# Kernel tuning notes

Hardware: AMD Instinct MI355X
Metric: run time of the kernel (lower is better)

## Reference

```python
import jax, jax.numpy as jnp
import numpy as np

D_MODEL = 2048
N_HEADS = 16
D_K = D_MODEL // N_HEADS
BATCH = 2
SEQ = 2048


def _rope(q, k):
    # q,k: [B, H, S, Dk], interleaved even/odd RoPE as in the torch source
    seq_len = q.shape[2]
    d = q.shape[-1]
    freqs = 1.0 / (10000.0 ** (jnp.arange(0, d, 2.0, dtype=jnp.float32) / d))  # [Dk/2]
    pos = jnp.arange(seq_len, dtype=jnp.float32)
    ang = pos[:, None] * freqs[None, :]          # [S, Dk/2]
    sin, cos = jnp.sin(ang), jnp.cos(ang)

    def rot(t):
        te, to = t[..., ::2], t[..., 1::2]
        out = jnp.stack([te * cos - to * sin, te * sin + to * cos], axis=-1)
        return out.reshape(t.shape)

    return rot(q), rot(k)


def setup_inputs() -> dict:
    key = jax.random.key(0)
    ks = jax.random.split(key, 5)
    scale = 1.0 / np.sqrt(D_MODEL)
    return {
        "x": jax.random.normal(ks[0], (BATCH, SEQ, D_MODEL), jnp.float32),
        "w_q": jax.random.normal(ks[1], (D_MODEL, D_MODEL), jnp.float32) * scale,
        "w_k": jax.random.normal(ks[2], (D_MODEL, D_MODEL), jnp.float32) * scale,
        "w_v": jax.random.normal(ks[3], (D_MODEL, D_MODEL), jnp.float32) * scale,
        "w_o": jax.random.normal(ks[4], (D_MODEL, D_MODEL), jnp.float32) * scale,
        "b_o": jnp.zeros((D_MODEL,), jnp.float32),
    }


def reference(x, w_q, w_k, w_v, w_o, b_o):
    B, S, D = x.shape
    H, Dk = N_HEADS, D_K
    # nn.Linear: y = x @ W.T
    q = (x @ w_q.T).reshape(B, S, H, Dk).transpose(0, 2, 1, 3)
    k = (x @ w_k.T).reshape(B, S, H, Dk).transpose(0, 2, 1, 3)
    v = (x @ w_v.T).reshape(B, S, H, Dk).transpose(0, 2, 1, 3)
    q, k = _rope(q, k)
    scores = jnp.einsum('bhqd,bhkd->bhqk', q, k) / jnp.sqrt(jnp.float32(Dk))
    causal = jnp.tril(jnp.ones((S, S), bool))  # True = keep
    scores = jnp.where(causal[None, None], scores, -jnp.inf)
    attn = jax.nn.softmax(scores, axis=-1)
    out = jnp.einsum('bhqk,bhkd->bhqd', attn, v)
    out = out.transpose(0, 2, 1, 3).reshape(B, S, D)
    return out @ w_o.T + b_o
```

## Files before the change

### kernel.cpp

```cpp
#include <hip/hip_runtime.h>

#define D_MODEL 2048
#define NHEADS  16
#define DK      128
#define BATCH   2
#define SEQ     2048
#define MTOT    (BATCH*SEQ)

typedef unsigned short u16;
typedef unsigned int   u32;
typedef __bf16 bf16x8 __attribute__((ext_vector_type(8)));
typedef float  f32x4  __attribute__((ext_vector_type(4)));

__device__ __forceinline__ float b2f(u16 u) {
  return __uint_as_float(((u32)u) << 16);
}
__device__ __forceinline__ u16 f2b(float f) {
  u32 x = __float_as_uint(f);
  x += 0x7fffu + ((x >> 16) & 1u);
  return (u16)(x >> 16);
}

__device__ __forceinline__ void gl2lds16(const u16* g, u16* l) {
  __builtin_amdgcn_global_load_lds(
      (const __attribute__((address_space(1))) void*)g,
      (__attribute__((address_space(3))) void*)l, 16, 0, 0);
}

__global__ __launch_bounds__(256) void cvt_k(const float* __restrict__ in,
                                             u16* __restrict__ out, int n4) {
  int i = blockIdx.x * 256 + threadIdx.x;
  if (i >= n4) return;
  float4 v = ((const float4*)in)[i];
  u32 lo = (u32)f2b(v.x) | ((u32)f2b(v.y) << 16);
  u32 hi = (u32)f2b(v.z) | ((u32)f2b(v.w) << 16);
  ((uint2*)out)[i] = make_uint2(lo, hi);
}

__global__ __launch_bounds__(256) void cvt4_k(const float* __restrict__ a, const float* __restrict__ b,
                                              const float* __restrict__ c, const float* __restrict__ d,
                                              u16* __restrict__ oa, u16* __restrict__ ob,
                                              u16* __restrict__ oc, u16* __restrict__ od, int n4) {
  int z = blockIdx.y;
  const float* in = (z == 0) ? a : (z == 1) ? b : (z == 2) ? c : d;
  u16* out = (z == 0) ? oa : (z == 1) ? ob : (z == 2) ? oc : od;
  int i = blockIdx.x * 256 + threadIdx.x;
  if (i >= n4) return;
  float4 v = ((const float4*)in)[i];
  u32 lo = (u32)f2b(v.x) | ((u32)f2b(v.y) << 16);
  u32 hi = (u32)f2b(v.z) | ((u32)f2b(v.w) << 16);
  ((uint2*)out)[i] = make_uint2(lo, hi);
}

__global__ __launch_bounds__(512, 2) void gemm256(const u16* __restrict__ A,
                                                  const u16* __restrict__ B,
                                                  const int M, const int N, const int K,
                                                  u16* __restrict__ outb,
                                                  float* __restrict__ outf,
                                                  const float* __restrict__ bias,
                                                  const int mode) {
  __shared__ __align__(16) u16 smem[3 * 24576];

  const int t    = threadIdx.x;
  const int lane = t & 63;
  const int wave = t >> 6;
  const int wm   = wave >> 1, wn = wave & 1;
  const int quad = lane >> 4, l16 = lane & 15;
  const int m0 = blockIdx.y * 256, n0 = blockIdx.x * 128;
  const int sr = lane & 15, sc = lane >> 4;

  const u16* agp[4]; u16* ald[4];
  const u16* bgp[2]; u16* bld[2];
#pragma unroll
  for (int q = 0; q < 4; ++q) {
    int a = wave * 4 + q;
    int kc = a >> 4, mt = a & 15;
    agp[q] = A + (size_t)(m0 + mt * 16 + sr) * K + kc * 32 + sc * 8;
    ald[q] = smem + a * 512;
  }
#pragma unroll
  for (int q = 0; q < 2; ++q) {
    int b = wave * 2 + q;
    int kc = b >> 3, nt = b & 7;
    bgp[q] = B + (size_t)(n0 + nt * 16 + sr) * K + kc * 32 + sc * 8;
    bld[q] = smem + 16384 + b * 512;
  }

  f32x4 acc[4][4] = {};
  const int NT = K >> 6;

#pragma unroll
  for (int q = 0; q < 4; ++q) { gl2lds16(agp[q], ald[q]);         agp[q] += 64; }
#pragma unroll
  for (int q = 0; q < 2; ++q) { gl2lds16(bgp[q], bld[q]);         bgp[q] += 64; }
#pragma unroll
  for (int q = 0; q < 4; ++q) { gl2lds16(agp[q], ald[q] + 24576); agp[q] += 64; }
#pragma unroll
  for (int q = 0; q < 2; ++q) { gl2lds16(bgp[q], bld[q] + 24576); bgp[q] += 64; }

  int cur = 0;
  for (int tt = 0; tt < NT; ++tt) {
    if (tt + 1 < NT) asm volatile("s_waitcnt vmcnt(6)" ::: "memory");
    else             asm volatile("s_waitcnt vmcnt(0)" ::: "memory");
    __builtin_amdgcn_s_barrier();
    asm volatile("" ::: "memory");

    if (tt + 2 < NT) {
      int nb = cur + 2; if (nb >= 3) nb -= 3;
      const int off = nb * 24576;
#pragma unroll
      for (int q = 0; q < 4; ++q) { gl2lds16(agp[q], ald[q] + off); agp[q] += 64; }
#pragma unroll
      for (int q = 0; q < 2; ++q) { gl2lds16(bgp[q], bld[q] + off); bgp[q] += 64; }
    }

    const u16* As = smem + cur * 24576;
    const u16* Bs = As + 16384;
#pragma unroll
    for (int kc = 0; kc < 2; ++kc) {
      bf16x8 af[4], bfv[4];
#pragma unroll
      for (int i = 0; i < 4; ++i)
        af[i] = *(const bf16x8*)&As[(kc * 16 + wm * 4 + i) * 512 + lane * 8];
#pragma unroll
      for (int j = 0; j < 4; ++j)
        bfv[j] = *(const bf16x8*)&Bs[(kc * 8 + wn * 4 + j) * 512 + lane * 8];
      __builtin_amdgcn_s_setprio(1);
#pragma unroll
      for (int i = 0; i < 4; ++i)
#pragma unroll
        for (int j = 0; j < 4; ++j)
          acc[i][j] = __builtin_amdgcn_mfma_f32_16x16x32_bf16(af[i], bfv[j], acc[i][j], 0, 0, 0);
      __builtin_amdgcn_s_setprio(0);
    }
    asm volatile("" ::: "memory");
    __builtin_amdgcn_s_barrier();
    cur = cur + 1; if (cur >= 3) cur -= 3;
  }

  if (mode == 0) {
#pragma unroll
    for (int i = 0; i < 4; ++i)
#pragma unroll
      for (int j = 0; j < 4; ++j)
#pragma unroll
        for (int rr = 0; rr < 4; ++rr) {
          int row = m0 + wm * 64 + i * 16 + quad * 4 + rr;
          int col = n0 + wn * 64 + j * 16 + l16;
          outf[(size_t)row * N + col] = acc[i][j][rr] + bias[col];
        }
  } else {
    const int tens = n0 >> 11;
    const int h    = (n0 & 2047) >> 7;
    const bool doRope = (tens < 2);
    const float mult = (tens == 0) ? 0.08838834764831845f : 1.0f;
#pragma unroll
    for (int j = 0; j < 4; ++j) {
      const int d = wn * 64 + j * 16 + l16;
      const float freq = exp2f(-0.20762050593045951f * (float)(d >> 1));
      const float sgn  = (d & 1) ? 1.f : -1.f;
#pragma unroll
      for (int i = 0; i < 4; ++i)
#pragma unroll
        for (int rr = 0; rr < 4; ++rr) {
          int row = m0 + wm * 64 + i * 16 + quad * 4 + rr;
          int b = row >> 11;
          int s = row & (SEQ - 1);
          float v = acc[i][j][rr];
          if (doRope) {
            float sn, cs;
            __sincosf((float)s * freq, &sn, &cs);
            float pv = __shfl_xor(v, 1);
            v = (v * cs + sgn * pv * sn) * mult;
          }
          outb[(size_t)tens * 8388608 + (((size_t)(b * NHEADS + h)) * SEQ + s) * DK + d] = f2b(v);
        }
    }
  }
}

__global__ __launch_bounds__(256) void vt_k(const u16* __restrict__ V,
                                            u16* __restrict__ Vt) {
  constexpr int LDT = 72;
  __shared__ __align__(16) u16 tile[64 * LDT];
  const int s0 = blockIdx.x * 64, d0 = blockIdx.y * 64, bh = blockIdx.z;
  const u16* in = V + (size_t)bh * SEQ * DK;
  u16* out = Vt + (size_t)bh * DK * SEQ;
  const int t = threadIdx.x;
  const int r = t >> 3, cg = t & 7;
#pragma unroll
  for (int half = 0; half < 2; ++half) {
    uint4 v = *(const uint4*)(in + (size_t)(s0 + r + half * 32) * DK + d0 + cg * 8);
    *(uint4*)&tile[(r + half * 32) * LDT + cg * 8] = v;
  }
  __syncthreads();
#pragma unroll
  for (int half = 0; half < 2; ++half) {
    int d = (t >> 3) + half * 32;
    __align__(16) u16 tmp[8];
#pragma unroll
    for (int i = 0; i < 8; ++i) tmp[i] = tile[(cg * 8 + i) * LDT + d];
    *(uint4*)(out + (size_t)(d0 + d) * SEQ + s0 + cg * 8) = *(const uint4*)tmp;
  }
}

__global__ __launch_bounds__(256, 4) void attn_k(const u16* __restrict__ Q,
                                                 const u16* __restrict__ K,
                                                 const u16* __restrict__ Vt,
                                                 u16* __restrict__ out) {
  __shared__ __align__(16) u16 smem[8192 + 8192 + 4096];
  u16* Ks = smem;
  u16* Vs = smem + 8192;

  const int t    = threadIdx.x;
  const int lane = t & 63;
  const int wave = t >> 6;
  const int quad = lane >> 4, l16 = lane & 15;
  u16* Psw = smem + 16384 + wave * 1024;
  const int pmask = (l16 & 7) << 3;
  const int qt = (int)gridDim.x - 1 - (int)blockIdx.x;
  const int bh = blockIdx.y;
  const size_t baseQK = (size_t)bh * SEQ * DK;
  const size_t baseV  = (size_t)bh * DK * SEQ;
  const int qw = qt * 64 + wave * 16;
  const int qglob = qw + l16;

  bf16x8 qf[4];
#pragma unroll
  for (int kc = 0; kc < 4; ++kc)
    qf[kc] = *(const bf16x8*)(Q + baseQK + (size_t)(qw + l16) * DK + kc * 32 + quad * 8);

  f32x4 oacc[8] = {};
  float m_run = -1e30f, l_run = 0.f;

  const int sr = lane & 15, sc = lane >> 4;
  const u16* kp[4]; u16* kd[4];
  const u16* vp[4]; u16* vd[4];
#pragma unroll
  for (int j = 0; j < 4; ++j) {
    int lin = wave * 4 + j;
    int knt = lin >> 2, kkc = lin & 3;
    kp[j] = K + baseQK + (size_t)(knt * 16 + sr) * DK + kkc * 32 + sc * 8;
    kd[j] = Ks + lin * 512;
    int vkc = lin >> 3, vnt = lin & 7;
    vp[j] = Vt + baseV + (size_t)(vnt * 16 + sr) * SEQ + vkc * 32 + sc * 8;
    vd[j] = Vs + lin * 512;
  }

  const int kend = (qt + 1) * 64;
  for (int k0 = 0; k0 < kend; k0 += 64) {
    __syncthreads();
#pragma unroll
    for (int j = 0; j < 4; ++j) gl2lds16(kp[j], kd[j]);
#pragma unroll
    for (int j = 0; j < 4; ++j) gl2lds16(vp[j], vd[j]);
#pragma unroll
    for (int j = 0; j < 4; ++j) { kp[j] += (size_t)64 * DK; vp[j] += 64; }
    __syncthreads();

    if (k0 >= qw + 16) continue;

    f32x4 s[4] = {};
#pragma unroll
    for (int kc = 0; kc < 4; ++kc) {
#pragma unroll
      for (int nt = 0; nt < 4; ++nt) {
        bf16x8 kf = *(const bf16x8*)&Ks[(nt * 4 + kc) * 512 + lane * 8];
        s[nt] = __builtin_amdgcn_mfma_f32_16x16x32_bf16(kf, qf[kc], s[nt], 0, 0, 0);
      }
    }

    float p[4][4];
    float newm = m_run;
    if (k0 + 63 > qw) {
#pragma unroll
      for (int nt = 0; nt < 4; ++nt)
#pragma unroll
        for (int r = 0; r < 4; ++r) {
          int key = k0 + nt * 16 + quad * 4 + r;
          float v = (key <= qglob) ? s[nt][r] : -1e30f;
          p[nt][r] = v;
          newm = fmaxf(newm, v);
        }
    } else {
#pragma unroll
      for (int nt = 0; nt < 4; ++nt)
#pragma unroll
        for (int r = 0; r < 4; ++r) {
          p[nt][r] = s[nt][r];
          newm = fmaxf(newm, s[nt][r]);
        }
    }
    newm = fmaxf(newm, __shfl_xor(newm, 16));
    newm = fmaxf(newm, __shfl_xor(newm, 32));
    float lsum = 0.f;
#pragma unroll
    for (int nt = 0; nt < 4; ++nt)
#pragma unroll
      for (int r = 0; r < 4; ++r) {
        float e = __expf(p[nt][r] - newm);
        p[nt][r] = e;
        lsum += e;
      }
    lsum += __shfl_xor(lsum, 16);
    lsum += __shfl_xor(lsum, 32);
    float alpha = __expf(m_run - newm);
    l_run = l_run * alpha + lsum;
    m_run = newm;

#pragma unroll
    for (int nt = 0; nt < 4; ++nt) {
      u32 lo = (u32)f2b(p[nt][0]) | ((u32)f2b(p[nt][1]) << 16);
      u32 hi = (u32)f2b(p[nt][2]) | ((u32)f2b(p[nt][3]) << 16);
      *(uint2*)&Psw[l16 * 64 + ((nt * 16 + quad * 4) ^ pmask)] = make_uint2(lo, hi);
    }

#pragma unroll
    for (int r = 0; r < 4; ++r) {
      float av = __shfl(alpha, quad * 4 + r);
#pragma unroll
      for (int nt = 0; nt < 8; ++nt) oacc[nt][r] *= av;
    }

#pragma unroll
    for (int kcp = 0; kcp < 2; ++kcp) {
      bf16x8 pf = *(const bf16x8*)&Psw[l16 * 64 + ((kcp * 32 + quad * 8) ^ pmask)];
#pragma unroll
      for (int nt = 0; nt < 8; ++nt) {
        bf16x8 vf = *(const bf16x8*)&Vs[(kcp * 8 + nt) * 512 + lane * 8];
        oacc[nt] = __builtin_amdgcn_mfma_f32_16x16x32_bf16(pf, vf, oacc[nt], 0, 0, 0);
      }
    }
  }

  constexpr int LDO = 136;
  float invl = 1.f / l_run;
  __syncthreads();
#pragma unroll
  for (int r = 0; r < 4; ++r) {
    float iv = __shfl(invl, quad * 4 + r);
#pragma unroll
    for (int nt = 0; nt < 8; ++nt)
      smem[(wave * 16 + quad * 4 + r) * LDO + nt * 16 + l16] = f2b(oacc[nt][r] * iv);
  }
  __syncthreads();
  const int b = bh >> 4, h = bh & 15;
#pragma unroll
  for (int pss = 0; pss < 4; ++pss) {
    int row = (t >> 4) + pss * 16;
    uint4 v = *(const uint4*)&smem[row * LDO + (t & 15) * 8];
    *(uint4*)(out + ((size_t)(b * SEQ + qt * 64 + row)) * D_MODEL + h * DK + (t & 15) * 8) = v;
  }
}

extern "C" void kernel_launch(void* const* d_in, const int* in_sizes, int n_in,
                              void* d_out, int out_size, void* d_ws, size_t ws_size,
                              hipStream_t stream) {
  const float* x  = (const float*)d_in[0];
  const float* wq = (const float*)d_in[1];
  const float* wk = (const float*)d_in[2];
  const float* wv = (const float*)d_in[3];
  const float* wo = (const float*)d_in[4];
  const float* bo = (const float*)d_in[5];
  float* out = (float*)d_out;

  char* wsb = (char*)d_ws;
  u16* xb    = (u16*)(wsb + 0);
  u16* wqb   = (u16*)(wsb + 16777216);
  u16* wkb   = (u16*)(wsb + 25165824);
  u16* wvb   = (u16*)(wsb + 33554432);
  u16* wob   = (u16*)(wsb + 41943040);
  u16* Qb    = (u16*)(wsb + 50331648);
  u16* Kb    = (u16*)(wsb + 67108864);
  u16* Vb    = (u16*)(wsb + 83886080);
  u16* attnb = xb;
  u16* Vtb   = wqb;

  cvt_k<<<8192, 256, 0, stream>>>(x, xb, MTOT * D_MODEL / 4);
  cvt4_k<<<dim3(4096, 4), 256, 0, stream>>>(wq, wk, wv, wo, wqb, wkb, wvb, wob,
                                            D_MODEL * D_MODEL / 4);

  gemm256<<<dim3(48, 16), 512, 0, stream>>>(xb, wqb, MTOT, 3 * D_MODEL, D_MODEL,
                                            Qb, nullptr, nullptr, 1);

  vt_k<<<dim3(SEQ / 64, DK / 64, BATCH * NHEADS), 256, 0, stream>>>(Vb, Vtb);

  attn_k<<<dim3(SEQ / 64, BATCH * NHEADS), 256, 0, stream>>>(Qb, Kb, Vtb, attnb);

  gemm256<<<dim3(16, 16), 512, 0, stream>>>(attnb, wob, MTOT, D_MODEL, D_MODEL,
                                            nullptr, out, bo, 0);
}
```

Before: 492.4 us.

## Switch GEMM to double-buffered half-tile pipeline with split K-chunk loads

Replaces the triple-buffered 64-wide K staging in the bf16 GEMM with a two-buffer scheme that loads and consumes each 32-wide K half separately. Each half-step issues the global-to-LDS loads for the next half right after reading fragments from LDS. Explicit barriers and lgkmcnt waits separate the LDS reads from the MFMA blocks. This cuts LDS use from 144KB to 96KB per block and overlaps copies at finer granularity, at the cost of twice as many barriers per K step and a shallower prefetch distance.

New measurement: 492.9 us. No clear change (+0.1%).

```diff
diff --git a/kernel.cpp b/kernel.cpp
--- a/kernel.cpp
+++ b/kernel.cpp
@@ -59,7 +59,7 @@
                                                   float* __restrict__ outf,
                                                   const float* __restrict__ bias,
                                                   const int mode) {
-  __shared__ __align__(16) u16 smem[3 * 24576];
+  __shared__ __align__(16) u16 smem[2 * 24576];
 
   const int t    = threadIdx.x;
   const int lane = t & 63;
@@ -69,73 +69,87 @@
   const int m0 = blockIdx.y * 256, n0 = blockIdx.x * 128;
   const int sr = lane & 15, sc = lane >> 4;
 
-  const u16* agp[4]; u16* ald[4];
-  const u16* bgp[2]; u16* bld[2];
-#pragma unroll
-  for (int q = 0; q < 4; ++q) {
-    int a = wave * 4 + q;
-    int kc = a >> 4, mt = a & 15;
-    agp[q] = A + (size_t)(m0 + mt * 16 + sr) * K + kc * 32 + sc * 8;
-    ald[q] = smem + a * 512;
-  }
-#pragma unroll
-  for (int q = 0; q < 2; ++q) {
-    int b = wave * 2 + q;
-    int kc = b >> 3, nt = b & 7;
-    bgp[q] = B + (size_t)(n0 + nt * 16 + sr) * K + kc * 32 + sc * 8;
-    bld[q] = smem + 16384 + b * 512;
-  }
+  const u16* aP[2][2]; u32 aOff[2][2];
+  const u16* bP[2];    u32 bOff[2];
+#pragma unroll
+  for (int kc = 0; kc < 2; ++kc) {
+#pragma unroll
+    for (int q = 0; q < 2; ++q) {
+      int mt = wave * 2 + q;
+      aP[kc][q]  = A + (size_t)(m0 + mt * 16 + sr) * K + kc * 32 + sc * 8;
+      aOff[kc][q] = (u32)(kc * 16 + mt) * 512;
+    }
+    bP[kc]  = B + (size_t)(n0 + wave * 16 + sr) * K + kc * 32 + sc * 8;
+    bOff[kc] = 16384u + (u32)(kc * 8 + wave) * 512;
+  }
+
+  auto issueHalf = [&](int kc, int buf) {
+    u16* base = smem + buf * 24576;
+    gl2lds16(aP[kc][0], base + aOff[kc][0]); aP[kc][0] += 64;
+    gl2lds16(aP[kc][1], base + aOff[kc][1]); aP[kc][1] += 64;
+    gl2lds16(bP[kc],    base + bOff[kc]);    bP[kc]    += 64;
+  };
 
   f32x4 acc[4][4] = {};
   const int NT = K >> 6;
 
-#pragma unroll
-  for (int q = 0; q < 4; ++q) { gl2lds16(agp[q], ald[q]);         agp[q] += 64; }
-#pragma unroll
-  for (int q = 0; q < 2; ++q) { gl2lds16(bgp[q], bld[q]);         bgp[q] += 64; }
-#pragma unroll
-  for (int q = 0; q < 4; ++q) { gl2lds16(agp[q], ald[q] + 24576); agp[q] += 64; }
-#pragma unroll
-  for (int q = 0; q < 2; ++q) { gl2lds16(bgp[q], bld[q] + 24576); bgp[q] += 64; }
-
-  int cur = 0;
+  issueHalf(0, 0);
+  issueHalf(1, 0);
+  issueHalf(0, 1);
+  asm volatile("s_waitcnt vmcnt(3)" ::: "memory");
+  __builtin_amdgcn_s_barrier();
+
   for (int tt = 0; tt < NT; ++tt) {
-    if (tt + 1 < NT) asm volatile("s_waitcnt vmcnt(6)" ::: "memory");
-    else             asm volatile("s_waitcnt vmcnt(0)" ::: "memory");
-    __builtin_amdgcn_s_barrier();
-    asm volatile("" ::: "memory");
-
-    if (tt + 2 < NT) {
-      int nb = cur + 2; if (nb >= 3) nb -= 3;
-      const int off = nb * 24576;
-#pragma unroll
-      for (int q = 0; q < 4; ++q) { gl2lds16(agp[q], ald[q] + off); agp[q] += 64; }
-#pragma unroll
-      for (int q = 0; q < 2; ++q) { gl2lds16(bgp[q], bld[q] + off); bgp[q] += 64; }
-    }
-
-    const u16* As = smem + cur * 24576;
+    const int cb = tt & 1;
+    const u16* As = smem + cb * 24576;
     const u16* Bs = As + 16384;
-#pragma unroll
-    for (int kc = 0; kc < 2; ++kc) {
-      bf16x8 af[4], bfv[4];
-#pragma unroll
-      for (int i = 0; i < 4; ++i)
-        af[i] = *(const bf16x8*)&As[(kc * 16 + wm * 4 + i) * 512 + lane * 8];
-#pragma unroll
-      for (int j = 0; j < 4; ++j)
-        bfv[j] = *(const bf16x8*)&Bs[(kc * 8 + wn * 4 + j) * 512 + lane * 8];
-      __builtin_amdgcn_s_setprio(1);
-#pragma unroll
-      for (int i = 0; i < 4; ++i)
-#pragma unroll
-        for (int j = 0; j < 4; ++j)
-          acc[i][j] = __builtin_amdgcn_mfma_f32_16x16x32_bf16(af[i], bfv[j], acc[i][j], 0, 0, 0);
-      __builtin_amdgcn_s_setprio(0);
-    }
+
+    bf16x8 af[4], bfv[4];
+#pragma unroll
+    for (int i = 0; i < 4; ++i)
+      af[i] = *(const bf16x8*)&As[(wm * 4 + i) * 512 + lane * 8];
+#pragma unroll
+    for (int j = 0; j < 4; ++j)
+      bfv[j] = *(const bf16x8*)&Bs[(wn * 4 + j) * 512 + lane * 8];
+    if (tt + 1 < NT) issueHalf(1, cb ^ 1);
     asm volatile("" ::: "memory");
     __builtin_amdgcn_s_barrier();
-    cur = cur + 1; if (cur >= 3) cur -= 3;
+    asm volatile("s_waitcnt lgkmcnt(0)" ::: "memory");
+    __builtin_amdgcn_sched_barrier(0);
+    __builtin_amdgcn_s_setprio(1);
+#pragma unroll
+    for (int i = 0; i < 4; ++i)
+#pragma unroll
+      for (int j = 0; j < 4; ++j)
+        acc[i][j] = __builtin_amdgcn_mfma_f32_16x16x32_bf16(af[i], bfv[j], acc[i][j], 0, 0, 0);
+    __builtin_amdgcn_s_setprio(0);
+    asm volatile("" ::: "memory");
+    __builtin_amdgcn_s_barrier();
+
+#pragma unroll
+    for (int i = 0; i < 4; ++i)
+      af[i] = *(const bf16x8*)&As[(16 + wm * 4 + i) * 512 + lane * 8];
+#pragma unroll
+    for (int j = 0; j < 4; ++j)
+      bfv[j] = *(const bf16x8*)&Bs[(8 + wn * 4 + j) * 512 + lane * 8];
+    if (tt + 2 < NT) issueHalf(0, cb);
+    if (tt + 1 < NT) {
+      if (tt + 2 < NT) asm volatile("s_waitcnt vmcnt(3)" ::: "memory");
+      else             asm volatile("s_waitcnt vmcnt(0)" ::: "memory");
+    }
+    asm volatile("" ::: "memory");
+    __builtin_amdgcn_s_barrier();
+    asm volatile("s_waitcnt lgkmcnt(0)" ::: "memory");
+    __builtin_amdgcn_sched_barrier(0);
+    __builtin_amdgcn_s_setprio(1);
+#pragma unroll
+    for (int i = 0; i < 4; ++i)
+#pragma unroll
+      for (int j = 0; j < 4; ++j)
+        acc[i][j] = __builtin_amdgcn_mfma_f32_16x16x32_bf16(af[i], bfv[j], acc[i][j], 0, 0, 0);
+    __builtin_amdgcn_s_setprio(0);
+    asm volatile("" ::: "memory");
+    __builtin_amdgcn_s_barrier();
   }
 
   if (mode == 0) {
```

## Enlarge GEMM tile to 256x256 with double-buffered, interleaved load/MFMA schedule

Applied to the files above, without the earlier changes.

The bf16 GEMM block tile grows from 256x128 to 256x256, with 8 waves arranged 2x4 and each wave holding 8x4 accumulators. The triple-buffered LDS pipeline becomes a double buffer whose global-to-LDS loads for the next tile are spread across four MFMA phases, with barriers and setprio between them. The aim is more reuse per LDS load and hiding of global-load latency. The cost is twice as many accumulator registers and far fewer blocks: 384 for the QKV projection and only 128 for the output projection, which may underfill the GPU's CUs.

New measurement: 532.3 us. +8.1%, slower.

```diff
diff --git a/kernel.cpp b/kernel.cpp
--- a/kernel.cpp
+++ b/kernel.cpp
@@ -59,111 +59,156 @@
                                                   float* __restrict__ outf,
                                                   const float* __restrict__ bias,
                                                   const int mode) {
-  __shared__ __align__(16) u16 smem[3 * 24576];
+  __shared__ __align__(16) u16 smem[65536];
 
   const int t    = threadIdx.x;
   const int lane = t & 63;
   const int wave = t >> 6;
-  const int wm   = wave >> 1, wn = wave & 1;
+  const int wm   = wave >> 2, wn = wave & 3;
   const int quad = lane >> 4, l16 = lane & 15;
-  const int m0 = blockIdx.y * 256, n0 = blockIdx.x * 128;
+  const int m0 = blockIdx.y * 256, n0 = blockIdx.x * 256;
   const int sr = lane & 15, sc = lane >> 4;
 
-  const u16* agp[4]; u16* ald[4];
-  const u16* bgp[2]; u16* bld[2];
+  const u16* aSrc[4]; u32 aDst[4];
+  const u16* bSrc[4]; u32 bDst[4];
 #pragma unroll
   for (int q = 0; q < 4; ++q) {
-    int a = wave * 4 + q;
-    int kc = a >> 4, mt = a & 15;
-    agp[q] = A + (size_t)(m0 + mt * 16 + sr) * K + kc * 32 + sc * 8;
-    ald[q] = smem + a * 512;
-  }
-#pragma unroll
-  for (int q = 0; q < 2; ++q) {
-    int b = wave * 2 + q;
-    int kc = b >> 3, nt = b & 7;
-    bgp[q] = B + (size_t)(n0 + nt * 16 + sr) * K + kc * 32 + sc * 8;
-    bld[q] = smem + 16384 + b * 512;
-  }
-
-  f32x4 acc[4][4] = {};
+    int id = q * 8 + wave;
+    int kc = id >> 4, t16 = id & 15;
+    aSrc[q] = A + (size_t)(m0 + t16 * 16 + sr) * K + kc * 32 + sc * 8;
+    aDst[q] = (u32)id * 512;
+    bSrc[q] = B + (size_t)(n0 + t16 * 16 + sr) * K + kc * 32 + sc * 8;
+    bDst[q] = 16384u + (u32)id * 512;
+  }
+
+  f32x4 acc[8][4] = {};
   const int NT = K >> 6;
 
 #pragma unroll
-  for (int q = 0; q < 4; ++q) { gl2lds16(agp[q], ald[q]);         agp[q] += 64; }
-#pragma unroll
-  for (int q = 0; q < 2; ++q) { gl2lds16(bgp[q], bld[q]);         bgp[q] += 64; }
-#pragma unroll
-  for (int q = 0; q < 4; ++q) { gl2lds16(agp[q], ald[q] + 24576); agp[q] += 64; }
-#pragma unroll
-  for (int q = 0; q < 2; ++q) { gl2lds16(bgp[q], bld[q] + 24576); bgp[q] += 64; }
-
-  int cur = 0;
+  for (int q = 0; q < 4; ++q) {
+    gl2lds16(aSrc[q], smem + aDst[q]); aSrc[q] += 64;
+    gl2lds16(bSrc[q], smem + bDst[q]); bSrc[q] += 64;
+  }
+
   for (int tt = 0; tt < NT; ++tt) {
-    if (tt + 1 < NT) asm volatile("s_waitcnt vmcnt(6)" ::: "memory");
-    else             asm volatile("s_waitcnt vmcnt(0)" ::: "memory");
-    __builtin_amdgcn_s_barrier();
-    asm volatile("" ::: "memory");
-
-    if (tt + 2 < NT) {
-      int nb = cur + 2; if (nb >= 3) nb -= 3;
-      const int off = nb * 24576;
-#pragma unroll
-      for (int q = 0; q < 4; ++q) { gl2lds16(agp[q], ald[q] + off); agp[q] += 64; }
-#pragma unroll
-      for (int q = 0; q < 2; ++q) { gl2lds16(bgp[q], bld[q] + off); bgp[q] += 64; }
-    }
-
-    const u16* As = smem + cur * 24576;
-    const u16* Bs = As + 16384;
-#pragma unroll
-    for (int kc = 0; kc < 2; ++kc) {
-      bf16x8 af[4], bfv[4];
-#pragma unroll
-      for (int i = 0; i < 4; ++i)
-        af[i] = *(const bf16x8*)&As[(kc * 16 + wm * 4 + i) * 512 + lane * 8];
+    u16* bufC = smem + (tt & 1) * 32768;
+    u16* bufN = smem + ((tt & 1) ^ 1) * 32768;
+    const bool more = (tt + 1 < NT);
+
+    if (more) {
+      gl2lds16(aSrc[0], bufN + aDst[0]); aSrc[0] += 64;
+      gl2lds16(bSrc[0], bufN + bDst[0]); bSrc[0] += 64;
+      asm volatile("s_waitcnt vmcnt(2)" ::: "memory");
+    } else {
+      asm volatile("s_waitcnt vmcnt(0)" ::: "memory");
+    }
+    __builtin_amdgcn_s_barrier();
+
+    const u16* Ab = bufC;
+    const u16* Bb = bufC + 16384;
+    bf16x8 af[4], bfv[4];
+
+#pragma unroll
+    for (int ii = 0; ii < 4; ++ii)
+      af[ii] = *(const bf16x8*)&Ab[(u32)(wm * 8 + ii) * 512 + lane * 8];
+#pragma unroll
+    for (int j = 0; j < 4; ++j)
+      bfv[j] = *(const bf16x8*)&Bb[(u32)(wn * 4 + j) * 512 + lane * 8];
+    if (more) {
+      gl2lds16(aSrc[1], bufN + aDst[1]); aSrc[1] += 64;
+      gl2lds16(bSrc[1], bufN + bDst[1]); bSrc[1] += 64;
+      gl2lds16(aSrc[2], bufN + aDst[2]); aSrc[2] += 64;
+      gl2lds16(bSrc[2], bufN + bDst[2]); bSrc[2] += 64;
+    }
+    __builtin_amdgcn_s_barrier();
+    asm volatile("s_waitcnt lgkmcnt(0)" ::: "memory");
+    __builtin_amdgcn_s_setprio(1);
+#pragma unroll
+    for (int ii = 0; ii < 4; ++ii)
 #pragma unroll
       for (int j = 0; j < 4; ++j)
-        bfv[j] = *(const bf16x8*)&Bs[(kc * 8 + wn * 4 + j) * 512 + lane * 8];
-      __builtin_amdgcn_s_setprio(1);
-#pragma unroll
-      for (int i = 0; i < 4; ++i)
-#pragma unroll
-        for (int j = 0; j < 4; ++j)
-          acc[i][j] = __builtin_amdgcn_mfma_f32_16x16x32_bf16(af[i], bfv[j], acc[i][j], 0, 0, 0);
-      __builtin_amdgcn_s_setprio(0);
-    }
-    asm volatile("" ::: "memory");
-    __builtin_amdgcn_s_barrier();
-    cur = cur + 1; if (cur >= 3) cur -= 3;
+        acc[ii][j] = __builtin_amdgcn_mfma_f32_16x16x32_bf16(af[ii], bfv[j], acc[ii][j], 0, 0, 0);
+    __builtin_amdgcn_s_setprio(0);
+    __builtin_amdgcn_s_barrier();
+
+#pragma unroll
+    for (int ii = 0; ii < 4; ++ii)
+      af[ii] = *(const bf16x8*)&Ab[(u32)(wm * 8 + 4 + ii) * 512 + lane * 8];
+    if (more) {
+      gl2lds16(aSrc[3], bufN + aDst[3]); aSrc[3] += 64;
+      gl2lds16(bSrc[3], bufN + bDst[3]); bSrc[3] += 64;
+    }
+    __builtin_amdgcn_s_barrier();
+    asm volatile("s_waitcnt lgkmcnt(0)" ::: "memory");
+    __builtin_amdgcn_s_setprio(1);
+#pragma unroll
+    for (int ii = 0; ii < 4; ++ii)
+#pragma unroll
+      for (int j = 0; j < 4; ++j)
+        acc[ii + 4][j] = __builtin_amdgcn_mfma_f32_16x16x32_bf16(af[ii], bfv[j], acc[ii + 4][j], 0, 0, 0);
+    __builtin_amdgcn_s_setprio(0);
+    __builtin_amdgcn_s_barrier();
+
+#pragma unroll
+    for (int ii = 0; ii < 4; ++ii)
+      af[ii] = *(const bf16x8*)&Ab[(u32)(16 + wm * 8 + ii) * 512 + lane * 8];
+#pragma unroll
+    for (int j = 0; j < 4; ++j)
+      bfv[j] = *(const bf16x8*)&Bb[(u32)(16 + wn * 4 + j) * 512 + lane * 8];
+    __builtin_amdgcn_s_barrier();
+    asm volatile("s_waitcnt lgkmcnt(0)" ::: "memory");
+    __builtin_amdgcn_s_setprio(1);
+#pragma unroll
+    for (int ii = 0; ii < 4; ++ii)
+#pragma unroll
+      for (int j = 0; j < 4; ++j)
+        acc[ii][j] = __builtin_amdgcn_mfma_f32_16x16x32_bf16(af[ii], bfv[j], acc[ii][j], 0, 0, 0);
+    __builtin_amdgcn_s_setprio(0);
+    __builtin_amdgcn_s_barrier();
+
+#pragma unroll
+    for (int ii = 0; ii < 4; ++ii)
+      af[ii] = *(const bf16x8*)&Ab[(u32)(16 + wm * 8 + 4 + ii) * 512 + lane * 8];
+    __builtin_amdgcn_s_barrier();
+    asm volatile("s_waitcnt lgkmcnt(0)" ::: "memory");
+    __builtin_amdgcn_s_setprio(1);
+#pragma unroll
+    for (int ii = 0; ii < 4; ++ii)
+#pragma unroll
+      for (int j = 0; j < 4; ++j)
+        acc[ii + 4][j] = __builtin_amdgcn_mfma_f32_16x16x32_bf16(af[ii], bfv[j], acc[ii + 4][j], 0, 0, 0);
+    __builtin_amdgcn_s_setprio(0);
+    __builtin_amdgcn_s_barrier();
   }
 
   if (mode == 0) {
 #pragma unroll
-    for (int i = 0; i < 4; ++i)
+    for (int i = 0; i < 8; ++i)
 #pragma unroll
       for (int j = 0; j < 4; ++j)
 #pragma unroll
         for (int rr = 0; rr < 4; ++rr) {
-          int row = m0 + wm * 64 + i * 16 + quad * 4 + rr;
+          int row = m0 + wm * 128 + i * 16 + quad * 4 + rr;
           int col = n0 + wn * 64 + j * 16 + l16;
           outf[(size_t)row * N + col] = acc[i][j][rr] + bias[col];
         }
   } else {
-    const int tens = n0 >> 11;
-    const int h    = (n0 & 2047) >> 7;
+    const int hcol = n0 + wn * 64;
+    const int tens = hcol >> 11;
+    const int h    = (hcol >> 7) & 15;
+    const int db   = hcol & 127;
     const bool doRope = (tens < 2);
     const float mult = (tens == 0) ? 0.08838834764831845f : 1.0f;
 #pragma unroll
     for (int j = 0; j < 4; ++j) {
-      const int d = wn * 64 + j * 16 + l16;
+      const int d = db + j * 16 + l16;
       const float freq = exp2f(-0.20762050593045951f * (float)(d >> 1));
       const float sgn  = (d & 1) ? 1.f : -1.f;
 #pragma unroll
-      for (int i = 0; i < 4; ++i)
+      for (int i = 0; i < 8; ++i)
 #pragma unroll
         for (int rr = 0; rr < 4; ++rr) {
-          int row = m0 + wm * 64 + i * 16 + quad * 4 + rr;
+          int row = m0 + wm * 128 + i * 16 + quad * 4 + rr;
           int b = row >> 11;
           int s = row & (SEQ - 1);
           float v = acc[i][j][rr];
@@ -380,13 +425,13 @@
   cvt4_k<<<dim3(4096, 4), 256, 0, stream>>>(wq, wk, wv, wo, wqb, wkb, wvb, wob,
                                             D_MODEL * D_MODEL / 4);
 
-  gemm256<<<dim3(48, 16), 512, 0, stream>>>(xb, wqb, MTOT, 3 * D_MODEL, D_MODEL,
+  gemm256<<<dim3(24, 16), 512, 0, stream>>>(xb, wqb, MTOT, 3 * D_MODEL, D_MODEL,
                                             Qb, nullptr, nullptr, 1);
 
   vt_k<<<dim3(SEQ / 64, DK / 64, BATCH * NHEADS), 256, 0, stream>>>(Vb, Vtb);
 
   attn_k<<<dim3(SEQ / 64, BATCH * NHEADS), 256, 0, stream>>>(Qb, Kb, Vtb, attnb);
 
-  gemm256<<<dim3(16, 16), 512, 0, stream>>>(attnb, wob, MTOT, D_MODEL, D_MODEL,
-                                            nullptr, out, bo, 0);
-}
+  gemm256<<<dim3(8, 16), 512, 0, stream>>>(attnb, wob, MTOT, D_MODEL, D_MODEL,
+                                           nullptr, out, bo, 0);
+}
```

## Double-buffer K/V tiles in attention with async global-to-LDS prefetch

Applied to the files above, without the earlier changes.

The attention kernel now keeps two LDS buffers for the K and V tiles and issues the global-to-LDS loads for the next tile before computing on the current one. It waits with explicit vmcnt counts and raw barriers so memory latency overlaps the MFMA and softmax work. The loop also raises wave priority around the MFMA sections. LDS use roughly doubles and launch bounds drop from 4 to 2 blocks per CU, which risks lower occupancy.

New measurement: 505.0 us. 2.6% more time.

```diff
diff --git a/kernel.cpp b/kernel.cpp
--- a/kernel.cpp
+++ b/kernel.cpp
@@ -204,19 +204,17 @@
   }
 }
 
-__global__ __launch_bounds__(256, 4) void attn_k(const u16* __restrict__ Q,
+__global__ __launch_bounds__(256, 2) void attn_k(const u16* __restrict__ Q,
                                                  const u16* __restrict__ K,
                                                  const u16* __restrict__ Vt,
                                                  u16* __restrict__ out) {
-  __shared__ __align__(16) u16 smem[8192 + 8192 + 4096];
-  u16* Ks = smem;
-  u16* Vs = smem + 8192;
+  __shared__ __align__(16) u16 smem[40960];
 
   const int t    = threadIdx.x;
   const int lane = t & 63;
   const int wave = t >> 6;
   const int quad = lane >> 4, l16 = lane & 15;
-  u16* Psw = smem + 16384 + wave * 1024;
+  u16* Psw = smem + 32768 + wave * 1024;
   const int pmask = (l16 & 7) << 3;
   const int qt = (int)gridDim.x - 1 - (int)blockIdx.x;
   const int bh = blockIdx.y;
@@ -234,103 +232,121 @@
   float m_run = -1e30f, l_run = 0.f;
 
   const int sr = lane & 15, sc = lane >> 4;
-  const u16* kp[4]; u16* kd[4];
-  const u16* vp[4]; u16* vd[4];
+  const u16* kp[4]; u32 kdo[4];
+  const u16* vp[4]; u32 vdo[4];
 #pragma unroll
   for (int j = 0; j < 4; ++j) {
     int lin = wave * 4 + j;
     int knt = lin >> 2, kkc = lin & 3;
     kp[j] = K + baseQK + (size_t)(knt * 16 + sr) * DK + kkc * 32 + sc * 8;
-    kd[j] = Ks + lin * 512;
+    kdo[j] = (u32)lin * 512;
     int vkc = lin >> 3, vnt = lin & 7;
     vp[j] = Vt + baseV + (size_t)(vnt * 16 + sr) * SEQ + vkc * 32 + sc * 8;
-    vd[j] = Vs + lin * 512;
-  }
-
-  const int kend = (qt + 1) * 64;
-  for (int k0 = 0; k0 < kend; k0 += 64) {
-    __syncthreads();
-#pragma unroll
-    for (int j = 0; j < 4; ++j) gl2lds16(kp[j], kd[j]);
-#pragma unroll
-    for (int j = 0; j < 4; ++j) gl2lds16(vp[j], vd[j]);
-#pragma unroll
-    for (int j = 0; j < 4; ++j) { kp[j] += (size_t)64 * DK; vp[j] += 64; }
-    __syncthreads();
-
-    if (k0 >= qw + 16) continue;
-
-    f32x4 s[4] = {};
-#pragma unroll
-    for (int kc = 0; kc < 4; ++kc) {
+    vdo[j] = 16384u + (u32)lin * 512;
+  }
+
+  const int ntiles = qt + 1;
+#pragma unroll
+  for (int j = 0; j < 4; ++j) { gl2lds16(kp[j], smem + kdo[j]); kp[j] += (size_t)64 * DK; }
+#pragma unroll
+  for (int j = 0; j < 4; ++j) { gl2lds16(vp[j], smem + vdo[j]); vp[j] += 64; }
+
+  for (int tt = 0; tt < ntiles; ++tt) {
+    const int cb = tt & 1;
+    if (tt + 1 < ntiles) {
+      const u32 nb = (u32)(cb ^ 1) * 8192;
+#pragma unroll
+      for (int j = 0; j < 4; ++j) { gl2lds16(kp[j], smem + nb + kdo[j]); kp[j] += (size_t)64 * DK; }
+#pragma unroll
+      for (int j = 0; j < 4; ++j) { gl2lds16(vp[j], smem + nb + vdo[j]); vp[j] += 64; }
+      asm volatile("s_waitcnt vmcnt(8)" ::: "memory");
+    } else {
+      asm volatile("s_waitcnt vmcnt(0)" ::: "memory");
+    }
+    __builtin_amdgcn_s_barrier();
+
+    const int k0 = tt * 64;
+    if (k0 < qw + 16) {
+      const u16* Ks = smem + cb * 8192;
+      const u16* Vs = smem + 16384 + cb * 8192;
+
+      f32x4 s[4] = {};
+      __builtin_amdgcn_s_setprio(1);
+#pragma unroll
+      for (int kc = 0; kc < 4; ++kc) {
+#pragma unroll
+        for (int nt = 0; nt < 4; ++nt) {
+          bf16x8 kf = *(const bf16x8*)&Ks[(nt * 4 + kc) * 512 + lane * 8];
+          s[nt] = __builtin_amdgcn_mfma_f32_16x16x32_bf16(kf, qf[kc], s[nt], 0, 0, 0);
+        }
+      }
+      __builtin_amdgcn_s_setprio(0);
+
+      float p[4][4];
+      float newm = m_run;
+      if (k0 + 63 > qw) {
+#pragma unroll
+        for (int nt = 0; nt < 4; ++nt)
+#pragma unroll
+          for (int r = 0; r < 4; ++r) {
+            int key = k0 + nt * 16 + quad * 4 + r;
+            float v = (key <= qglob) ? s[nt][r] : -1e30f;
+            p[nt][r] = v;
+            newm = fmaxf(newm, v);
+          }
+      } else {
+#pragma unroll
+        for (int nt = 0; nt < 4; ++nt)
+#pragma unroll
+          for (int r = 0; r < 4; ++r) {
+            p[nt][r] = s[nt][r];
+            newm = fmaxf(newm, s[nt][r]);
+          }
+      }
+      newm = fmaxf(newm, __shfl_xor(newm, 16));
+      newm = fmaxf(newm, __shfl_xor(newm, 32));
+      float lsum = 0.f;
+#pragma unroll
+      for (int nt = 0; nt < 4; ++nt)
+#pragma unroll
+        for (int r = 0; r < 4; ++r) {
+          float e = __expf(p[nt][r] - newm);
+          p[nt][r] = e;
+          lsum += e;
+        }
+      lsum += __shfl_xor(lsum, 16);
+      lsum += __shfl_xor(lsum, 32);
+      float alpha = __expf(m_run - newm);
+      l_run = l_run * alpha + lsum;
+      m_run = newm;
+
 #pragma unroll
       for (int nt = 0; nt < 4; ++nt) {
-        bf16x8 kf = *(const bf16x8*)&Ks[(nt * 4 + kc) * 512 + lane * 8];
-        s[nt] = __builtin_amdgcn_mfma_f32_16x16x32_bf16(kf, qf[kc], s[nt], 0, 0, 0);
+        u32 lo = (u32)f2b(p[nt][0]) | ((u32)f2b(p[nt][1]) << 16);
+        u32 hi = (u32)f2b(p[nt][2]) | ((u32)f2b(p[nt][3]) << 16);
+        *(uint2*)&Psw[l16 * 64 + ((nt * 16 + quad * 4) ^ pmask)] = make_uint2(lo, hi);
       }
+
+#pragma unroll
+      for (int r = 0; r < 4; ++r) {
+        float av = __shfl(alpha, quad * 4 + r);
+#pragma unroll
+        for (int nt = 0; nt < 8; ++nt) oacc[nt][r] *= av;
+      }
+
+      __builtin_amdgcn_s_setprio(1);
+#pragma unroll
+      for (int kcp = 0; kcp < 2; ++kcp) {
+        bf16x8 pf = *(const bf16x8*)&Psw[l16 * 64 + ((kcp * 32 + quad * 8) ^ pmask)];
+#pragma unroll
+        for (int nt = 0; nt < 8; ++nt) {
+          bf16x8 vf = *(const bf16x8*)&Vs[(kcp * 8 + nt) * 512 + lane * 8];
+          oacc[nt] = __builtin_amdgcn_mfma_f32_16x16x32_bf16(pf, vf, oacc[nt], 0, 0, 0);
+        }
+      }
+      __builtin_amdgcn_s_setprio(0);
     }
-
-    float p[4][4];
-    float newm = m_run;
-    if (k0 + 63 > qw) {
-#pragma unroll
-      for (int nt = 0; nt < 4; ++nt)
-#pragma unroll
-        for (int r = 0; r < 4; ++r) {
-          int key = k0 + nt * 16 + quad * 4 + r;
-          float v = (key <= qglob) ? s[nt][r] : -1e30f;
-          p[nt][r] = v;
-          newm = fmaxf(newm, v);
-        }
-    } else {
-#pragma unroll
-      for (int nt = 0; nt < 4; ++nt)
-#pragma unroll
-        for (int r = 0; r < 4; ++r) {
-          p[nt][r] = s[nt][r];
-          newm = fmaxf(newm, s[nt][r]);
-        }
-    }
-    newm = fmaxf(newm, __shfl_xor(newm, 16));
-    newm = fmaxf(newm, __shfl_xor(newm, 32));
-    float lsum = 0.f;
-#pragma unroll
-    for (int nt = 0; nt < 4; ++nt)
-#pragma unroll
-      for (int r = 0; r < 4; ++r) {
-        float e = __expf(p[nt][r] - newm);
-        p[nt][r] = e;
-        lsum += e;
-      }
-    lsum += __shfl_xor(lsum, 16);
-    lsum += __shfl_xor(lsum, 32);
-    float alpha = __expf(m_run - newm);
-    l_run = l_run * alpha + lsum;
-    m_run = newm;
-
-#pragma unroll
-    for (int nt = 0; nt < 4; ++nt) {
-      u32 lo = (u32)f2b(p[nt][0]) | ((u32)f2b(p[nt][1]) << 16);
-      u32 hi = (u32)f2b(p[nt][2]) | ((u32)f2b(p[nt][3]) << 16);
-      *(uint2*)&Psw[l16 * 64 + ((nt * 16 + quad * 4) ^ pmask)] = make_uint2(lo, hi);
-    }
-
-#pragma unroll
-    for (int r = 0; r < 4; ++r) {
-      float av = __shfl(alpha, quad * 4 + r);
-#pragma unroll
-      for (int nt = 0; nt < 8; ++nt) oacc[nt][r] *= av;
-    }
-
-#pragma unroll
-    for (int kcp = 0; kcp < 2; ++kcp) {
-      bf16x8 pf = *(const bf16x8*)&Psw[l16 * 64 + ((kcp * 32 + quad * 8) ^ pmask)];
-#pragma unroll
-      for (int nt = 0; nt < 8; ++nt) {
-        bf16x8 vf = *(const bf16x8*)&Vs[(kcp * 8 + nt) * 512 + lane * 8];
-        oacc[nt] = __builtin_amdgcn_mfma_f32_16x16x32_bf16(pf, vf, oacc[nt], 0, 0, 0);
-      }
-    }
+    __builtin_amdgcn_s_barrier();
   }
 
   constexpr int LDO = 136;
```
